# Kernel optimization log

Hardware: AMD Instinct MI355X
Metric: run time of the kernel (lower is better)

Reference implementation:

```python
import jax, jax.numpy as jnp
import numpy as np

P = 2        # patch_size
HEADS = 1


def _conv(x, w, b, groups=1):
    # NCHW conv, kernel 3x3, SAME padding (stride 1)
    y = jax.lax.conv_general_dilated(
        x, w, window_strides=(1, 1), padding='SAME',
        dimension_numbers=('NCHW', 'OIHW', 'NCHW'),
        feature_group_count=groups)
    return y + b[None, :, None, None]


def _unfold(x, p):
    # torch.nn.Unfold(kernel=p, stride=p): [B,C,h,w] -> [B, C*p*p, n]
    B, C, h, w = x.shape
    x = x.reshape(B, C, h // p, p, w // p, p)
    x = x.transpose(0, 1, 3, 5, 2, 4)  # (B, C, ph, pw, h/p, w/p)
    return x.reshape(B, C * p * p, (h // p) * (w // p))


def _fold(x, p, h, w):
    # inverse of _unfold (non-overlapping patches)
    B = x.shape[0]
    C = x.shape[1] // (p * p)
    x = x.reshape(B, C, p, p, h // p, w // p)
    x = x.transpose(0, 1, 4, 2, 5, 3)  # (B, C, h/p, ph, w/p, pw)
    return x.reshape(B, C, h, w)


def setup_inputs() -> dict:
    key = jax.random.key(0)
    ks = jax.random.split(key, 9)
    c = 64
    x = jax.random.normal(ks[0], (2, 5, c, 64, 64), jnp.float32)
    wq = jax.random.normal(ks[1], (c, 1, 3, 3), jnp.float32) * 0.1
    bq = jax.random.normal(ks[2], (c,), jnp.float32) * 0.1
    wk = jax.random.normal(ks[3], (c, 1, 3, 3), jnp.float32) * 0.1
    bk = jax.random.normal(ks[4], (c,), jnp.float32) * 0.1
    wv = jax.random.normal(ks[5], (c, c, 3, 3), jnp.float32) * 0.05
    bv = jax.random.normal(ks[6], (c,), jnp.float32) * 0.1
    wc = jax.random.normal(ks[7], (c, c, 3, 3), jnp.float32) * 0.05
    bc = jax.random.normal(ks[8], (c,), jnp.float32) * 0.1
    return {"x": x, "wq": wq, "bq": bq, "wk": wk, "bk": bk,
            "wv": wv, "bv": bv, "wc": wc, "bc": bc}


def reference(x, wq, bq, wk, bk, wv, bv, wc, bc):
    b, t, c, h, w = x.shape
    p, H = P, HEADS
    D = p * p * c           # 256
    d = D // H              # per-head dim
    n = (h // p) * (w // p)  # tokens per frame

    xf = x.reshape(b * t, c, h, w)
    q = _conv(xf, wq, bq, groups=c)   # depthwise
    k = _conv(xf, wk, bk, groups=c)   # depthwise
    v = _conv(xf, wv, bv)             # dense conv

    def to_tokens(y):
        # [bt, D, n] -> [b, H, d, t*n]
        u = _unfold(y, p).reshape(b, t, H, d, n)
        return u.transpose(0, 2, 3, 1, 4).reshape(b, H, d, t * n)

    uq, uk, uv = to_tokens(q), to_tokens(k), to_tokens(v)

    attn = jnp.einsum('bhdi,bhdj->bhij', uq, uk) * (d ** -0.5)
    attn = jax.nn.softmax(attn, axis=-1)           # [b,H,tn,tn]
    ax = jnp.einsum('bhij,bhdj->bhid', attn, uv)   # [b,H,tn,d]

    ax = ax.reshape(b, H, t, n, d).transpose(0, 2, 1, 4, 3).reshape(b * t, D, n)
    feat = _fold(ax, p, h, w)                      # [bt, c, h, w]
    out = _conv(feat, wc, bc).reshape(x.shape) + x
    return out
```

## Files before the change

### kernel.cpp

```cpp
#include <hip/hip_runtime.h>
#include <hip/hip_bf16.h>

typedef __attribute__((ext_vector_type(8))) short short8;
typedef __attribute__((ext_vector_type(8))) unsigned short ushort8;
typedef __attribute__((ext_vector_type(4))) unsigned short ushort4v;
typedef __attribute__((ext_vector_type(4))) float f32x4;

#define NTOK 5120
#define DDIM 256
#define NJC 8

__device__ __forceinline__ unsigned short f2bf(float f) {
  union { float f; unsigned int u; } x; x.f = f;
  unsigned int r = x.u + 0x7FFFu + ((x.u >> 16) & 1u);
  return (unsigned short)(r >> 16);
}
__device__ __forceinline__ float bf2f(unsigned short u) {
  union { unsigned int i; float f; } x; x.i = ((unsigned int)u) << 16; return x.f;
}

__global__ __launch_bounds__(256) void qk_gen(
    const float* __restrict__ xin, const float* __restrict__ wq,
    const float* __restrict__ bq, const float* __restrict__ wk,
    const float* __restrict__ bk, unsigned short* __restrict__ qt,
    unsigned short* __restrict__ kt)
{
  const int ch = blockIdx.x;
  const int bt = blockIdx.y;
  const int b = bt / 5, tf = bt % 5;
  const int tid = threadIdx.x;
  const float* xp = xin + ((size_t)bt * 64 + ch) * 4096;
  float wqv[9], wkv[9];
  #pragma unroll
  for (int i = 0; i < 9; i++) { wqv[i] = wq[ch * 9 + i]; wkv[i] = wk[ch * 9 + i]; }
  const float bqv = bq[ch], bkv = bk[ch];

  #pragma unroll
  for (int p = 0; p < 4; p++) {
    int pid = tid + p * 256;
    int gy = pid >> 5, gx = pid & 31;
    float v[4][4];
    #pragma unroll
    for (int r = 0; r < 4; r++) {
      int yy = 2 * gy - 1 + r;
      #pragma unroll
      for (int cc = 0; cc < 4; cc++) {
        int xx = 2 * gx - 1 + cc;
        bool ok = (yy >= 0) && (yy < 64) && (xx >= 0) && (xx < 64);
        v[r][cc] = ok ? xp[yy * 64 + xx] : 0.f;
      }
    }
    unsigned short qo[4], ko[4];
    #pragma unroll
    for (int py = 0; py < 2; py++)
      #pragma unroll
      for (int px = 0; px < 2; px++) {
        float aq = bqv, ak = bkv;
        #pragma unroll
        for (int dy = 0; dy < 3; dy++)
          #pragma unroll
          for (int dx = 0; dx < 3; dx++) {
            float xv = v[py + dy][px + dx];
            aq += wqv[dy * 3 + dx] * xv;
            ak += wkv[dy * 3 + dx] * xv;
          }
        qo[py * 2 + px] = f2bf(aq);
        ko[py * 2 + px] = f2bf(ak);
      }
    size_t base = ((size_t)(b * NTOK + tf * 1024 + pid)) * DDIM + ch * 4;
    ushort4v qv = { qo[0], qo[1], qo[2], qo[3] };
    ushort4v kv = { ko[0], ko[1], ko[2], ko[3] };
    *(ushort4v*)(qt + base) = qv;
    *(ushort4v*)(kt + base) = kv;
  }
}

__global__ __launch_bounds__(256) void wt_gen(
    const float* __restrict__ w0, const float* __restrict__ w1,
    unsigned short* __restrict__ o0, unsigned short* __restrict__ o1)
{
  const int tap = blockIdx.x;
  const float* src = blockIdx.y ? w1 : w0;
  unsigned short* dst = blockIdx.y ? o1 : o0;
  const int t = threadIdx.x;
  #pragma unroll
  for (int i = 0; i < 16; i++) {
    int oi = t + i * 256;
    dst[tap * 4096 + oi] = f2bf(src[(size_t)oi * 9 + tap]);
  }
}

template<int MODE>
__global__ __launch_bounds__(256) void conv_mfma(
    const float* __restrict__ src, const unsigned short* __restrict__ wt,
    const float* __restrict__ bias, const float* __restrict__ resid,
    float* __restrict__ dstf, unsigned short* __restrict__ vt)
{
  const int strip = blockIdx.x;
  const int bt = blockIdx.y;
  const int y0 = strip * 2;
  const int tid = threadIdx.x;
  const int sw = tid >> 6, lane = tid & 63;
  const int ry = sw >> 1, ch = sw & 1;
  const int g = lane >> 4, c = lane & 15;

  __shared__ __align__(16) unsigned short lds_in[4 * 66 * 64];
  __shared__ __align__(16) unsigned short lds_w[64 * 64];

  {
    const int rr = lane >> 4;
    const int cb = lane & 15;
    const int row = y0 - 1 + rr;
    const bool rok = (row >= 0) && (row < 64);
    #pragma unroll
    for (int pp = 0; pp < 8; ++pp) {
      const int ci0 = sw * 16 + pp * 2;
      f32x4 va = { 0.f, 0.f, 0.f, 0.f }, vb = { 0.f, 0.f, 0.f, 0.f };
      if (rok) {
        va = *(const f32x4*)(src + ((size_t)(bt * 64 + ci0)) * 4096 + row * 64 + cb * 4);
        vb = *(const f32x4*)(src + ((size_t)(bt * 64 + ci0 + 1)) * 4096 + row * 64 + cb * 4);
      }
      char* rbase = (char*)lds_in + (rr * 66) * 128 + (ci0 & 7) * 2;
      const int sl = ci0 >> 3;
      #pragma unroll
      for (int q = 0; q < 4; ++q) {
        int lcol = cb * 4 + q + 1;
        unsigned int pk = (unsigned int)f2bf(va[q]) | ((unsigned int)f2bf(vb[q]) << 16);
        *(unsigned int*)(rbase + lcol * 128 + ((sl ^ (lcol & 7)) * 16)) = pk;
      }
      if (cb == 0)  *(unsigned int*)(rbase + ((sl ^ 0) * 16)) = 0u;
      if (cb == 15) *(unsigned int*)(rbase + 65 * 128 + ((sl ^ 1) * 16)) = 0u;
    }
  }

  f32x4 acc[2][4];
  #pragma unroll
  for (int ct = 0; ct < 2; ct++)
    #pragma unroll
    for (int xt = 0; xt < 4; xt++) acc[ct][xt] = (f32x4){ 0.f, 0.f, 0.f, 0.f };

  #pragma unroll 1
  for (int tap = 0; tap < 9; ++tap) {
    __syncthreads();
    {
      const unsigned short* wp = wt + tap * 4096;
      #pragma unroll
      for (int h = 0; h < 2; ++h) {
        int el = h * 2048 + tid * 8;
        int co = el >> 6, sl = (el & 63) >> 3;
        short8 wv8 = *(const short8*)(wp + el);
        *(short8*)((char*)lds_w + co * 128 + ((sl ^ (co & 7)) * 16)) = wv8;
      }
    }
    __syncthreads();
    const int dy = tap / 3 - 1, dx = tap % 3 - 1;
    const int rowp = ry + 1 + dy;
    #pragma unroll
    for (int kblk = 0; kblk < 2; ++kblk) {
      short8 af[2], bf[4];
      #pragma unroll
      for (int ct = 0; ct < 2; ++ct) {
        int co = ch * 32 + ct * 16 + c;
        af[ct] = *(const short8*)((char*)lds_w + co * 128 + (((kblk * 4 + g) ^ (co & 7)) * 16));
      }
      #pragma unroll
      for (int xt = 0; xt < 4; ++xt) {
        int lcol = xt * 16 + c + dx + 1;
        bf[xt] = *(const short8*)((char*)lds_in + (rowp * 66 + lcol) * 128 + (((kblk * 4 + g) ^ (lcol & 7)) * 16));
      }
      #pragma unroll
      for (int ct = 0; ct < 2; ++ct)
        #pragma unroll
        for (int xt = 0; xt < 4; ++xt)
          acc[ct][xt] = __builtin_amdgcn_mfma_f32_16x16x32_bf16(af[ct], bf[xt], acc[ct][xt], 0, 0, 0);
    }
  }

  const int y = y0 + ry;
  if (MODE == 0) {
    const int b = bt / 5, tf = bt % 5;
    const int py = y & 1, gy = y >> 1;
    #pragma unroll
    for (int ct = 0; ct < 2; ++ct)
      #pragma unroll
      for (int r = 0; r < 4; ++r) {
        const int co = ch * 32 + ct * 16 + g * 4 + r;
        const float bv = bias[co];
        #pragma unroll
        for (int xt = 0; xt < 4; ++xt) {
          int x = xt * 16 + c;
          int d = co * 4 + py * 2 + (x & 1);
          int tok = tf * 1024 + gy * 32 + (x >> 1);
          vt[((size_t)(b * DDIM + d)) * NTOK + tok] = f2bf(acc[ct][xt][r] + bv);
        }
      }
  } else {
    #pragma unroll
    for (int ct = 0; ct < 2; ++ct)
      #pragma unroll
      for (int r = 0; r < 4; ++r) {
        const int co = ch * 32 + ct * 16 + g * 4 + r;
        const float bv = bias[co];
        const size_t rowb = ((size_t)(bt * 64 + co)) * 4096 + (size_t)y * 64;
        #pragma unroll
        for (int xt = 0; xt < 4; ++xt) {
          int x = xt * 16 + c;
          dstf[rowb + x] = acc[ct][xt][r] + bv + resid[rowb + x];
        }
      }
  }
}

__global__ __launch_bounds__(256) void attn_kernel(
    const unsigned short* __restrict__ qt, const unsigned short* __restrict__ kt,
    const unsigned short* __restrict__ vt, float* __restrict__ po,
    float* __restrict__ pm, float* __restrict__ pl)
{
  const int wgid = blockIdx.x;
  const int chunk = wgid / 320;
  const int within = wgid % 320;
  const int slice = chunk * 8 + (within & 7);
  const int b = slice >> 3;
  const int jc = slice & 7;
  const int i0 = (within >> 3) * 128;
  const int jchunk = NTOK / NJC;
  const int tid = threadIdx.x;
  const int w = tid >> 6, lane = tid & 63;
  const int g = lane >> 4, c = lane & 15;

  __shared__ __align__(16) unsigned short lds_k[64 * 256];
  __shared__ __align__(16) unsigned short lds_v[256 * 64];
  __shared__ __align__(16) unsigned short lds_p[4 * 16 * 64];

  short8 qf[2][8];
  #pragma unroll
  for (int st = 0; st < 2; st++) {
    const unsigned short* qr = qt + ((size_t)(b * NTOK + i0 + w * 32 + st * 16 + c)) * DDIM + g * 8;
    #pragma unroll
    for (int kb = 0; kb < 8; kb++) qf[st][kb] = *(const short8*)(qr + kb * 32);
  }
  f32x4 o[32];
  #pragma unroll
  for (int i = 0; i < 32; i++) o[i] = (f32x4){ 0.f, 0.f, 0.f, 0.f };
  float m[2][4], l[2][4];
  #pragma unroll
  for (int st = 0; st < 2; st++)
    #pragma unroll
    for (int r = 0; r < 4; r++) { m[st][r] = -1e30f; l[st][r] = 0.f; }

  const int sr = tid >> 5, sc = tid & 31;
  const int vdr = tid >> 3, vcc = tid & 7;
  char* pb = (char*)lds_p + w * 2048;

  const int jbeg = jc * jchunk;
  const int jend = jbeg + jchunk;

  short8 kpre[8], vpre[8];
  #pragma unroll
  for (int p = 0; p < 8; p++) {
    int row = sr + p * 8;
    kpre[p] = *(const short8*)(kt + ((size_t)(b * NTOK + jbeg + row)) * DDIM + sc * 8);
    int dd = vdr + p * 32;
    vpre[p] = *(const short8*)(vt + ((size_t)(b * DDIM + dd)) * NTOK + jbeg + vcc * 8);
  }

  for (int j0 = jbeg; j0 < jend; j0 += 64) {
    #pragma unroll
    for (int p = 0; p < 8; p++) {
      int row = sr + p * 8;
      *(short8*)((char*)lds_k + row * 512 + ((sc ^ (row & 7)) * 16)) = kpre[p];
      int dd = vdr + p * 32;
      *(short8*)((char*)lds_v + dd * 128 + ((vcc ^ (dd & 7)) * 16)) = vpre[p];
    }
    __syncthreads();

    if (j0 + 64 < jend) {
      const int jn = j0 + 64;
      #pragma unroll
      for (int p = 0; p < 8; p++) {
        int row = sr + p * 8;
        kpre[p] = *(const short8*)(kt + ((size_t)(b * NTOK + jn + row)) * DDIM + sc * 8);
        int dd = vdr + p * 32;
        vpre[p] = *(const short8*)(vt + ((size_t)(b * DDIM + dd)) * NTOK + jn + vcc * 8);
      }
    }

    f32x4 s0[4], s1[4];
    #pragma unroll
    for (int js = 0; js < 4; js++) {
      s0[js] = (f32x4){ 0.f, 0.f, 0.f, 0.f };
      s1[js] = (f32x4){ 0.f, 0.f, 0.f, 0.f };
      int row = js * 16 + c;
      int sw2 = row & 7;
      #pragma unroll
      for (int kb = 0; kb < 8; kb++) {
        short8 kf = *(const short8*)((char*)lds_k + row * 512 + (((kb * 4 + g) ^ sw2) * 16));
        s0[js] = __builtin_amdgcn_mfma_f32_16x16x32_bf16(qf[0][kb], kf, s0[js], 0, 0, 0);
        s1[js] = __builtin_amdgcn_mfma_f32_16x16x32_bf16(qf[1][kb], kf, s1[js], 0, 0, 0);
      }
    }
    short8 pf[2][2];
    {
      float pvv[4][4], alpha[4];
      int need = 0;
      #pragma unroll
      for (int r = 0; r < 4; r++) {
        float mx = fmaxf(fmaxf(s0[0][r], s0[1][r]), fmaxf(s0[2][r], s0[3][r])) * 0.0625f;
        #pragma unroll
        for (int off = 1; off < 16; off <<= 1) mx = fmaxf(mx, __shfl_xor(mx, off));
        float mold = m[0][r];
        float mn = fmaxf(mold, mx);
        alpha[r] = __expf(mold - mn);
        if (mn > mold) need = 1;
        float p0 = __expf(s0[0][r] * 0.0625f - mn);
        float p1 = __expf(s0[1][r] * 0.0625f - mn);
        float p2 = __expf(s0[2][r] * 0.0625f - mn);
        float p3 = __expf(s0[3][r] * 0.0625f - mn);
        pvv[0][r] = p0; pvv[1][r] = p1; pvv[2][r] = p2; pvv[3][r] = p3;
        float sum = p0 + p1 + p2 + p3;
        #pragma unroll
        for (int off = 1; off < 16; off <<= 1) sum += __shfl_xor(sum, off);
        l[0][r] = l[0][r] * alpha[r] + sum;
        m[0][r] = mn;
      }
      if (__any(need)) {
        f32x4 av = { alpha[0], alpha[1], alpha[2], alpha[3] };
        #pragma unroll
        for (int ds = 0; ds < 16; ds++) o[ds] *= av;
      }
      #pragma unroll
      for (int js = 0; js < 4; js++)
        #pragma unroll
        for (int r = 0; r < 4; r++) {
          int row = 4 * g + r;
          int slot = (js * 2 + (c >> 3)) ^ (row & 7);
          *(unsigned short*)(pb + row * 128 + slot * 16 + (c & 7) * 2) = f2bf(pvv[js][r]);
        }
      #pragma unroll
      for (int k2 = 0; k2 < 2; k2++)
        pf[0][k2] = *(short8*)(pb + c * 128 + (((k2 * 4 + g) ^ (c & 7)) * 16));
    }
    {
      float pvv[4][4], alpha[4];
      int need = 0;
      #pragma unroll
      for (int r = 0; r < 4; r++) {
        float mx = fmaxf(fmaxf(s1[0][r], s1[1][r]), fmaxf(s1[2][r], s1[3][r])) * 0.0625f;
        #pragma unroll
        for (int off = 1; off < 16; off <<= 1) mx = fmaxf(mx, __shfl_xor(mx, off));
        float mold = m[1][r];
        float mn = fmaxf(mold, mx);
        alpha[r] = __expf(mold - mn);
        if (mn > mold) need = 1;
        float p0 = __expf(s1[0][r] * 0.0625f - mn);
        float p1 = __expf(s1[1][r] * 0.0625f - mn);
        float p2 = __expf(s1[2][r] * 0.0625f - mn);
        float p3 = __expf(s1[3][r] * 0.0625f - mn);
        pvv[0][r] = p0; pvv[1][r] = p1; pvv[2][r] = p2; pvv[3][r] = p3;
        float sum = p0 + p1 + p2 + p3;
        #pragma unroll
        for (int off = 1; off < 16; off <<= 1) sum += __shfl_xor(sum, off);
        l[1][r] = l[1][r] * alpha[r] + sum;
        m[1][r] = mn;
      }
      if (__any(need)) {
        f32x4 av = { alpha[0], alpha[1], alpha[2], alpha[3] };
        #pragma unroll
        for (int ds = 0; ds < 16; ds++) o[16 + ds] *= av;
      }
      #pragma unroll
      for (int js = 0; js < 4; js++)
        #pragma unroll
        for (int r = 0; r < 4; r++) {
          int row = 4 * g + r;
          int slot = (js * 2 + (c >> 3)) ^ (row & 7);
          *(unsigned short*)(pb + row * 128 + slot * 16 + (c & 7) * 2) = f2bf(pvv[js][r]);
        }
      #pragma unroll
      for (int k2 = 0; k2 < 2; k2++)
        pf[1][k2] = *(short8*)(pb + c * 128 + (((k2 * 4 + g) ^ (c & 7)) * 16));
    }
    #pragma unroll
    for (int ds = 0; ds < 16; ds++) {
      int vrow = ds * 16 + c;
      int sw2 = c & 7;
      #pragma unroll
      for (int k2 = 0; k2 < 2; k2++) {
        short8 vf = *(const short8*)((char*)lds_v + vrow * 128 + (((k2 * 4 + g) ^ sw2) * 16));
        o[ds]      = __builtin_amdgcn_mfma_f32_16x16x32_bf16(pf[0][k2], vf, o[ds], 0, 0, 0);
        o[16 + ds] = __builtin_amdgcn_mfma_f32_16x16x32_bf16(pf[1][k2], vf, o[16 + ds], 0, 0, 0);
      }
    }
    __syncthreads();
  }
  #pragma unroll
  for (int st = 0; st < 2; st++) {
    const size_t rbase = ((size_t)(b * NJC + jc)) * NTOK + i0 + w * 32 + st * 16;
    #pragma unroll
    for (int ds = 0; ds < 16; ds++)
      #pragma unroll
      for (int r = 0; r < 4; r++)
        po[(rbase + 4 * g + r) * DDIM + ds * 16 + c] = o[st * 16 + ds][r];
    if (c == 0) {
      #pragma unroll
      for (int r = 0; r < 4; r++) {
        pm[rbase + 4 * g + r] = m[st][r];
        pl[rbase + 4 * g + r] = l[st][r];
      }
    }
  }
}

__global__ __launch_bounds__(256) void attn_combine(
    const float* __restrict__ po, const float* __restrict__ pm,
    const float* __restrict__ pl, float* __restrict__ feat, int njc)
{
  const int b = blockIdx.y;
  const int i0 = blockIdx.x * 64;
  const int t = threadIdx.x;
  const int row = t >> 2, dq = (t & 3) * 64;
  const int i = i0 + row;

  float M = -1e30f, L = 0.f;
  f32x4 acc[16];
  #pragma unroll
  for (int q = 0; q < 16; q++) acc[q] = (f32x4){ 0.f, 0.f, 0.f, 0.f };

  #pragma unroll 1
  for (int jc = 0; jc < njc; jc++) {
    const size_t rb = ((size_t)(b * njc + jc)) * NTOK + i;
    float mj = pm[rb], lj = pl[rb];
    float mn = fmaxf(M, mj);
    float so = __expf(M - mn), sn = __expf(mj - mn);
    const float* pp = po + rb * DDIM + dq;
    #pragma unroll
    for (int q = 0; q < 16; q++) {
      f32x4 v = *(const f32x4*)(pp + q * 4);
      acc[q] = acc[q] * so + v * sn;
    }
    L = L * so + lj * sn;
    M = mn;
  }
  const float inv = 1.f / L;
  const int tf = i >> 10, jn = i & 1023;
  const int gy = jn >> 5, gx = jn & 31;
  const size_t fb = ((size_t)((b * 5 + tf) * 64)) * 4096 + (2 * gy) * 64 + 2 * gx;
  #pragma unroll
  for (int q = 0; q < 16; q++) {
    f32x4 a = acc[q] * inv;
    int ch = (dq + q * 4) >> 2;
    size_t base = fb + (size_t)ch * 4096;
    feat[base] = a[0]; feat[base + 1] = a[1];
    feat[base + 64] = a[2]; feat[base + 65] = a[3];
  }
}

extern "C" void kernel_launch(void* const* d_in, const int* in_sizes, int n_in,
                              void* d_out, int out_size, void* d_ws, size_t ws_size,
                              hipStream_t stream) {
  const float* x  = (const float*)d_in[0];
  const float* wq = (const float*)d_in[1];
  const float* bq = (const float*)d_in[2];
  const float* wk = (const float*)d_in[3];
  const float* bk = (const float*)d_in[4];
  const float* wv = (const float*)d_in[5];
  const float* bv = (const float*)d_in[6];
  const float* wc = (const float*)d_in[7];
  const float* bc = (const float*)d_in[8];
  float* out = (float*)d_out;

  char* ws = (char*)d_ws;
  unsigned short* qt = (unsigned short*)(ws);
  unsigned short* kt = (unsigned short*)(ws + 5242880);
  unsigned short* vt = (unsigned short*)(ws + 10485760);
  float*          ft = (float*)(ws + 15728640);
  unsigned short* wtv = (unsigned short*)(ws + 26214400);
  unsigned short* wtc = (unsigned short*)(ws + 26288128);
  const size_t big_off = 26361856;
  float* po = (float*)(ws + big_off);

  size_t po_bytes = (size_t)2 * NJC * NTOK * DDIM * 4;
  float* pm = (float*)(ws + big_off + po_bytes);
  float* pl = pm + (size_t)2 * NJC * NTOK;

  wt_gen        <<<dim3(9, 2), 256, 0, stream>>>(wv, wc, wtv, wtc);
  qk_gen        <<<dim3(64, 10), 256, 0, stream>>>(x, wq, bq, wk, bk, qt, kt);
  conv_mfma<0>  <<<dim3(32, 10), 256, 0, stream>>>(x, wtv, bv, nullptr, nullptr, vt);
  attn_kernel   <<<dim3(640), 256, 0, stream>>>(qt, kt, vt, po, pm, pl);
  attn_combine  <<<dim3(80, 2), 256, 0, stream>>>(po, pm, pl, ft, NJC);
  conv_mfma<1>  <<<dim3(32, 10), 256, 0, stream>>>(ft, wtc, bc, x, out, nullptr);
}
```

Baseline: 283.3 us.

## Double-buffer K/V tiles in LDS and switch softmax to exp2 domain

The attention kernel now keeps two LDS buffers for the K and V tiles. It issues the global prefetch after the QK MFMAs and writes the next tile into the alternate buffer before the PV MFMAs, which drops one barrier per iteration and overlaps loads with compute. The softmax scale is folded with log2(e) so exp2f replaces __expf, and the merge kernel uses exp2f to match. The conditional rescale guarded by __any is removed, so the output accumulators are always rescaled. Doubling LDS to about 136 KB per block may lower occupancy.

```diff
diff --git a/kernel.cpp b/kernel.cpp
--- a/kernel.cpp
+++ b/kernel.cpp
@@ -228,9 +228,11 @@
   const int w = tid >> 6, lane = tid & 63;
   const int g = lane >> 4, c = lane & 15;
 
-  __shared__ __align__(16) unsigned short lds_k[64 * 256];
-  __shared__ __align__(16) unsigned short lds_v[256 * 64];
+  __shared__ __align__(16) unsigned short lds_k[2][64 * 256];
+  __shared__ __align__(16) unsigned short lds_v[2][256 * 64];
   __shared__ __align__(16) unsigned short lds_p[4 * 16 * 64];
+
+  const float C2 = 0.0625f * 1.4426950408889634f;
 
   short8 qf[2][8];
   #pragma unroll
@@ -255,26 +257,40 @@
   const int jbeg = jc * jchunk;
   const int jend = jbeg + jchunk;
 
-  short8 kpre[8], vpre[8];
-  #pragma unroll
-  for (int p = 0; p < 8; p++) {
-    int row = sr + p * 8;
-    kpre[p] = *(const short8*)(kt + ((size_t)(b * NTOK + jbeg + row)) * DDIM + sc * 8);
-    int dd = vdr + p * 32;
-    vpre[p] = *(const short8*)(vt + ((size_t)(b * DDIM + dd)) * NTOK + jbeg + vcc * 8);
-  }
-
-  for (int j0 = jbeg; j0 < jend; j0 += 64) {
+  {
     #pragma unroll
     for (int p = 0; p < 8; p++) {
       int row = sr + p * 8;
-      *(short8*)((char*)lds_k + row * 512 + ((sc ^ (row & 7)) * 16)) = kpre[p];
+      short8 kv = *(const short8*)(kt + ((size_t)(b * NTOK + jbeg + row)) * DDIM + sc * 8);
+      *(short8*)((char*)lds_k[0] + row * 512 + ((sc ^ (row & 7)) * 16)) = kv;
       int dd = vdr + p * 32;
-      *(short8*)((char*)lds_v + dd * 128 + ((vcc ^ (dd & 7)) * 16)) = vpre[p];
-    }
-    __syncthreads();
-
-    if (j0 + 64 < jend) {
+      short8 vv = *(const short8*)(vt + ((size_t)(b * DDIM + dd)) * NTOK + jbeg + vcc * 8);
+      *(short8*)((char*)lds_v[0] + dd * 128 + ((vcc ^ (dd & 7)) * 16)) = vv;
+    }
+  }
+  __syncthreads();
+
+  int cur = 0;
+  for (int j0 = jbeg; j0 < jend; j0 += 64) {
+    const bool more = (j0 + 64 < jend);
+
+    f32x4 s0[4], s1[4];
+    #pragma unroll
+    for (int js = 0; js < 4; js++) {
+      s0[js] = (f32x4){ 0.f, 0.f, 0.f, 0.f };
+      s1[js] = (f32x4){ 0.f, 0.f, 0.f, 0.f };
+      int row = js * 16 + c;
+      int sw2 = row & 7;
+      #pragma unroll
+      for (int kb = 0; kb < 8; kb++) {
+        short8 kf = *(const short8*)((char*)lds_k[cur] + row * 512 + (((kb * 4 + g) ^ sw2) * 16));
+        s0[js] = __builtin_amdgcn_mfma_f32_16x16x32_bf16(qf[0][kb], kf, s0[js], 0, 0, 0);
+        s1[js] = __builtin_amdgcn_mfma_f32_16x16x32_bf16(qf[1][kb], kf, s1[js], 0, 0, 0);
+      }
+    }
+
+    short8 kpre[8], vpre[8];
+    if (more) {
       const int jn = j0 + 64;
       #pragma unroll
       for (int p = 0; p < 8; p++) {
@@ -285,37 +301,21 @@
       }
     }
 
-    f32x4 s0[4], s1[4];
-    #pragma unroll
-    for (int js = 0; js < 4; js++) {
-      s0[js] = (f32x4){ 0.f, 0.f, 0.f, 0.f };
-      s1[js] = (f32x4){ 0.f, 0.f, 0.f, 0.f };
-      int row = js * 16 + c;
-      int sw2 = row & 7;
-      #pragma unroll
-      for (int kb = 0; kb < 8; kb++) {
-        short8 kf = *(const short8*)((char*)lds_k + row * 512 + (((kb * 4 + g) ^ sw2) * 16));
-        s0[js] = __builtin_amdgcn_mfma_f32_16x16x32_bf16(qf[0][kb], kf, s0[js], 0, 0, 0);
-        s1[js] = __builtin_amdgcn_mfma_f32_16x16x32_bf16(qf[1][kb], kf, s1[js], 0, 0, 0);
-      }
-    }
     short8 pf[2][2];
     {
       float pvv[4][4], alpha[4];
-      int need = 0;
       #pragma unroll
       for (int r = 0; r < 4; r++) {
-        float mx = fmaxf(fmaxf(s0[0][r], s0[1][r]), fmaxf(s0[2][r], s0[3][r])) * 0.0625f;
+        float t0 = s0[0][r] * C2, t1 = s0[1][r] * C2, t2 = s0[2][r] * C2, t3 = s0[3][r] * C2;
+        float mx = fmaxf(fmaxf(t0, t1), fmaxf(t2, t3));
         #pragma unroll
         for (int off = 1; off < 16; off <<= 1) mx = fmaxf(mx, __shfl_xor(mx, off));
-        float mold = m[0][r];
-        float mn = fmaxf(mold, mx);
-        alpha[r] = __expf(mold - mn);
-        if (mn > mold) need = 1;
-        float p0 = __expf(s0[0][r] * 0.0625f - mn);
-        float p1 = __expf(s0[1][r] * 0.0625f - mn);
-        float p2 = __expf(s0[2][r] * 0.0625f - mn);
-        float p3 = __expf(s0[3][r] * 0.0625f - mn);
+        float mn = fmaxf(m[0][r], mx);
+        alpha[r] = exp2f(m[0][r] - mn);
+        float p0 = exp2f(t0 - mn);
+        float p1 = exp2f(t1 - mn);
+        float p2 = exp2f(t2 - mn);
+        float p3 = exp2f(t3 - mn);
         pvv[0][r] = p0; pvv[1][r] = p1; pvv[2][r] = p2; pvv[3][r] = p3;
         float sum = p0 + p1 + p2 + p3;
         #pragma unroll
@@ -323,11 +323,9 @@
         l[0][r] = l[0][r] * alpha[r] + sum;
         m[0][r] = mn;
       }
-      if (__any(need)) {
-        f32x4 av = { alpha[0], alpha[1], alpha[2], alpha[3] };
-        #pragma unroll
-        for (int ds = 0; ds < 16; ds++) o[ds] *= av;
-      }
+      f32x4 av = { alpha[0], alpha[1], alpha[2], alpha[3] };
+      #pragma unroll
+      for (int ds = 0; ds < 16; ds++) o[ds] *= av;
       #pragma unroll
       for (int js = 0; js < 4; js++)
         #pragma unroll
@@ -342,20 +340,18 @@
     }
     {
       float pvv[4][4], alpha[4];
-      int need = 0;
       #pragma unroll
       for (int r = 0; r < 4; r++) {
-        float mx = fmaxf(fmaxf(s1[0][r], s1[1][r]), fmaxf(s1[2][r], s1[3][r])) * 0.0625f;
+        float t0 = s1[0][r] * C2, t1 = s1[1][r] * C2, t2 = s1[2][r] * C2, t3 = s1[3][r] * C2;
+        float mx = fmaxf(fmaxf(t0, t1), fmaxf(t2, t3));
         #pragma unroll
         for (int off = 1; off < 16; off <<= 1) mx = fmaxf(mx, __shfl_xor(mx, off));
-        float mold = m[1][r];
-        float mn = fmaxf(mold, mx);
-        alpha[r] = __expf(mold - mn);
-        if (mn > mold) need = 1;
-        float p0 = __expf(s1[0][r] * 0.0625f - mn);
-        float p1 = __expf(s1[1][r] * 0.0625f - mn);
-        float p2 = __expf(s1[2][r] * 0.0625f - mn);
-        float p3 = __expf(s1[3][r] * 0.0625f - mn);
+        float mn = fmaxf(m[1][r], mx);
+        alpha[r] = exp2f(m[1][r] - mn);
+        float p0 = exp2f(t0 - mn);
+        float p1 = exp2f(t1 - mn);
+        float p2 = exp2f(t2 - mn);
+        float p3 = exp2f(t3 - mn);
         pvv[0][r] = p0; pvv[1][r] = p1; pvv[2][r] = p2; pvv[3][r] = p3;
         float sum = p0 + p1 + p2 + p3;
         #pragma unroll
@@ -363,11 +359,9 @@
         l[1][r] = l[1][r] * alpha[r] + sum;
         m[1][r] = mn;
       }
-      if (__any(need)) {
-        f32x4 av = { alpha[0], alpha[1], alpha[2], alpha[3] };
-        #pragma unroll
-        for (int ds = 0; ds < 16; ds++) o[16 + ds] *= av;
-      }
+      f32x4 av = { alpha[0], alpha[1], alpha[2], alpha[3] };
+      #pragma unroll
+      for (int ds = 0; ds < 16; ds++) o[16 + ds] *= av;
       #pragma unroll
       for (int js = 0; js < 4; js++)
         #pragma unroll
@@ -380,18 +374,30 @@
       for (int k2 = 0; k2 < 2; k2++)
         pf[1][k2] = *(short8*)(pb + c * 128 + (((k2 * 4 + g) ^ (c & 7)) * 16));
     }
+
+    if (more) {
+      #pragma unroll
+      for (int p = 0; p < 8; p++) {
+        int row = sr + p * 8;
+        *(short8*)((char*)lds_k[cur ^ 1] + row * 512 + ((sc ^ (row & 7)) * 16)) = kpre[p];
+        int dd = vdr + p * 32;
+        *(short8*)((char*)lds_v[cur ^ 1] + dd * 128 + ((vcc ^ (dd & 7)) * 16)) = vpre[p];
+      }
+    }
+
     #pragma unroll
     for (int ds = 0; ds < 16; ds++) {
       int vrow = ds * 16 + c;
       int sw2 = c & 7;
       #pragma unroll
       for (int k2 = 0; k2 < 2; k2++) {
-        short8 vf = *(const short8*)((char*)lds_v + vrow * 128 + (((k2 * 4 + g) ^ sw2) * 16));
+        short8 vf = *(const short8*)((char*)lds_v[cur] + vrow * 128 + (((k2 * 4 + g) ^ sw2) * 16));
         o[ds]      = __builtin_amdgcn_mfma_f32_16x16x32_bf16(pf[0][k2], vf, o[ds], 0, 0, 0);
         o[16 + ds] = __builtin_amdgcn_mfma_f32_16x16x32_bf16(pf[1][k2], vf, o[16 + ds], 0, 0, 0);
       }
     }
     __syncthreads();
+    cur ^= 1;
   }
   #pragma unroll
   for (int st = 0; st < 2; st++) {
@@ -431,7 +437,7 @@
     const size_t rb = ((size_t)(b * njc + jc)) * NTOK + i;
     float mj = pm[rb], lj = pl[rb];
     float mn = fmaxf(M, mj);
-    float so = __expf(M - mn), sn = __expf(mj - mn);
+    float so = exp2f(M - mn), sn = exp2f(mj - mn);
     const float* pp = po + rb * DDIM + dq;
     #pragma unroll
     for (int q = 0; q < 16; q++) {
```

Result: faster. 270.6 us (-4.5%).
